# Performance work log

Hardware: AMD Instinct MI355X
Metric: run time of the kernel (lower is better)

The kernel has to match this reference:

```python
import jax, jax.numpy as jnp
import numpy as np

N = 50000   # input nodes per graph
M = 50000   # output nodes per graph
E = 1600000 # edges (avg degree 32)
B = 16      # batch size
D = 32      # Kaiming fan for init std


def setup_inputs() -> dict:
    key = jax.random.key(0)
    k1, k2, k3 = jax.random.split(key, 3)
    indices = jax.random.randint(k1, (2, E), 0, N, dtype=jnp.int64)  # row0=src in [0,N), row1=dst in [0,M)
    values = jax.random.normal(k2, (E,), dtype=jnp.float32) * (2.0 / D) ** 0.5
    bias = jnp.zeros((M, 1), dtype=jnp.float32)
    x = jax.random.normal(k3, (B, N, 1), dtype=jnp.float32)
    return {"x": x, "values": values, "bias": bias, "indices": indices}


def reference(x, values, bias, indices):
    # x: (B, N, 1); values: (E,); bias: (M, 1); indices: (2, E)
    # Equivalent to the PyG scatter-add message passing, but the block-diagonal
    # batched edge_index is never materialized: the sparsity pattern is shared
    # across the batch, so we gather once per batch via fancy indexing and
    # segment-sum over destination nodes.
    src, dst = indices[0], indices[1]
    msgs = x[:, src, 0] * values[None, :]                 # (B, E) gather-multiply
    agg = jax.ops.segment_sum(msgs.T, dst, num_segments=M)  # (M, B) scatter-add
    out = agg.T + bias[:, 0][None, :]                     # (B, M) bias add
    return out[..., None]                                  # (B, M, 1)
```

## Files before the change

kernel.cpp:

```cpp
#include <hip/hip_runtime.h>

#define E_EDGES 1600000
#define N_NODES 50000
#define M_NODES 50000
#define B_BATCH 16

#define RB         64
#define KB_BKT     782
#define TBLK       1024
#define NWG_T      49
#define NWG_B      512
#define CHUNK      3125
#define LD_ITERS   4
#define SLOT_CAP   8
#define BSPILL_CAP 64
#define PADR       73
#define ROW_CAP    72
#define SENT       0xFFFFFFFFu

__global__ void __launch_bounds__(TBLK) kAB6(
                     const float* __restrict__ x,
                     const int* __restrict__ idx,
                     const float* __restrict__ vals,
                     float4* __restrict__ xt,
                     float2* __restrict__ cells,
                     float2* __restrict__ bspill,
                     unsigned* __restrict__ scnt) {
    const int tid = threadIdx.x;
    if (blockIdx.x < NWG_T) {
        int n = blockIdx.x * TBLK + tid;
        if (n >= N_NODES) return;
        float v[B_BATCH];
#pragma unroll
        for (int b = 0; b < B_BATCH; ++b) v[b] = x[(size_t)b * N_NODES + n];
        float4* dst = xt + (size_t)n * 4;
#pragma unroll
        for (int j = 0; j < 4; ++j)
            dst[j] = make_float4(v[4*j], v[4*j+1], v[4*j+2], v[4*j+3]);
        return;
    }
    const int w = blockIdx.x - NWG_T;

    __shared__ unsigned cur[KB_BKT];
    __shared__ float2 cellbuf[KB_BKT * SLOT_CAP];

    for (int i = tid; i < KB_BKT; i += TBLK) cur[i] = 0;
    const float2 sent = make_float2(__uint_as_float(SENT), 0.f);
    for (int i = tid; i < KB_BKT * SLOT_CAP; i += TBLK) cellbuf[i] = sent;
    __syncthreads();

    const int base = w * CHUNK;
#pragma unroll
    for (int it = 0; it < LD_ITERS; ++it) {
        int li = it * TBLK + tid;
        if (li < CHUNK) {
            int e = base + li;
            unsigned s = (unsigned)idx[e];
            unsigned d = (unsigned)idx[E_EDGES + e];
            float v = vals[e];
            unsigned k = d >> 6;
            unsigned pack = s | (d << 16);
            unsigned p = atomicAdd(&cur[k], 1u);
            if (p < SLOT_CAP) {
                cellbuf[k * SLOT_CAP + p] = make_float2(__uint_as_float(pack), v);
            } else {
                unsigned sp = atomicAdd(&scnt[k], 1u);
                if (sp < BSPILL_CAP)
                    bspill[(size_t)k * BSPILL_CAP + sp] =
                        make_float2(__uint_as_float(pack), v);
            }
        }
    }
    __syncthreads();

    float4* cellsv4 = (float4*)cells;
    const float4* lbuf = (const float4*)cellbuf;
#pragma unroll
    for (int it2 = 0; it2 < 4; ++it2) {
        int kb = it2 * 256 + ((tid >> 6) << 4) + ((tid & 63) >> 2);
        int sub = tid & 3;
        if (kb < KB_BKT)
            cellsv4[((size_t)kb * NWG_B + w) * 4 + sub] = lbuf[kb * 4 + sub];
    }
}

__global__ void kC4(const float2* __restrict__ cells,
                    const float2* __restrict__ bspill,
                    const unsigned* __restrict__ scnt,
                    const float4* __restrict__ xt,
                    const float* __restrict__ bias,
                    float* __restrict__ out) {
    __shared__ float2 rowbuf[RB * PADR];
    __shared__ unsigned rcur[RB];
    __shared__ int oflow;
    __shared__ unsigned snum;

    const int tid = threadIdx.x;
    const int k = blockIdx.x;
    const int mbase = k * RB;

    if (tid < RB) rcur[tid] = 0;
    if (tid == 0) { oflow = 0; snum = scnt[k]; }
    __syncthreads();

    const float2* bkt = cells + (size_t)k * (NWG_B * SLOT_CAP);
    for (int i = tid; i < NWG_B * SLOT_CAP; i += 256) {
        float2 ed = bkt[i];
        unsigned u = __float_as_uint(ed.x);
        if (u != SENT) {
            unsigned r = (u >> 16) & 63u;
            unsigned q = atomicAdd(&rcur[r], 1u);
            if (q < ROW_CAP) rowbuf[r * PADR + q] = ed;
            else oflow = 1;
        }
    }
    __syncthreads();

    if (snum) {
        unsigned ns = (snum > BSPILL_CAP) ? BSPILL_CAP : snum;
        if ((unsigned)tid < ns) {
            float2 ed = bspill[(size_t)k * BSPILL_CAP + tid];
            unsigned r = (__float_as_uint(ed.x) >> 16) & 63u;
            unsigned q = atomicAdd(&rcur[r], 1u);
            if (q < ROW_CAP) rowbuf[r * PADR + q] = ed;
            else oflow = 1;
        }
        __syncthreads();
    }

    if (!oflow) {
        int r = tid >> 2;
        int quad = tid & 3;
        unsigned nr = rcur[r];
        const float2* row = &rowbuf[r * PADR];
        float4 acc = make_float4(0.f, 0.f, 0.f, 0.f);
        unsigned j = 0;
        for (; j + 1 < nr; j += 2) {
            float2 a = row[j];
            float2 b = row[j + 1];
            float4 xa = xt[(size_t)(__float_as_uint(a.x) & 0xFFFFu) * 4 + quad];
            float4 xb = xt[(size_t)(__float_as_uint(b.x) & 0xFFFFu) * 4 + quad];
            acc.x += xa.x * a.y; acc.y += xa.y * a.y;
            acc.z += xa.z * a.y; acc.w += xa.w * a.y;
            acc.x += xb.x * b.y; acc.y += xb.y * b.y;
            acc.z += xb.z * b.y; acc.w += xb.w * b.y;
        }
        if (j < nr) {
            float2 a = row[j];
            float4 xa = xt[(size_t)(__float_as_uint(a.x) & 0xFFFFu) * 4 + quad];
            acc.x += xa.x * a.y; acc.y += xa.y * a.y;
            acc.z += xa.z * a.y; acc.w += xa.w * a.y;
        }
        int m = mbase + r;
        if (m < M_NODES) {
            float bv = bias[m];
            out[(size_t)(quad * 4 + 0) * M_NODES + m] = acc.x + bv;
            out[(size_t)(quad * 4 + 1) * M_NODES + m] = acc.y + bv;
            out[(size_t)(quad * 4 + 2) * M_NODES + m] = acc.z + bv;
            out[(size_t)(quad * 4 + 3) * M_NODES + m] = acc.w + bv;
        }
    } else {
        __syncthreads();
        float* acc = (float*)rowbuf;
        for (int i = tid; i < B_BATCH * RB; i += 256) acc[i] = 0.f;
        __syncthreads();
        for (int i = tid; i < NWG_B * SLOT_CAP; i += 256) {
            float2 ed = bkt[i];
            unsigned u = __float_as_uint(ed.x);
            if (u != SENT) {
                int src = (int)(u & 0xFFFFu);
                int dl = (int)((u >> 16) & 63u);
                float v = ed.y;
                const float4* xr = xt + (size_t)src * 4;
                float4 a = xr[0], b4 = xr[1], cc = xr[2], d4 = xr[3];
                float xv[B_BATCH] = {a.x,a.y,a.z,a.w, b4.x,b4.y,b4.z,b4.w,
                                     cc.x,cc.y,cc.z,cc.w, d4.x,d4.y,d4.z,d4.w};
#pragma unroll
                for (int b = 0; b < B_BATCH; ++b)
                    atomicAdd(&acc[b * RB + dl], xv[b] * v);
            }
        }
        if (snum) {
            unsigned ns = (snum > BSPILL_CAP) ? BSPILL_CAP : snum;
            if ((unsigned)tid < ns) {
                float2 ed = bspill[(size_t)k * BSPILL_CAP + tid];
                unsigned u = __float_as_uint(ed.x);
                int src = (int)(u & 0xFFFFu);
                int dl = (int)((u >> 16) & 63u);
                float v = ed.y;
                const float4* xr = xt + (size_t)src * 4;
                float4 a = xr[0], b4 = xr[1], cc = xr[2], d4 = xr[3];
                float xv[B_BATCH] = {a.x,a.y,a.z,a.w, b4.x,b4.y,b4.z,b4.w,
                                     cc.x,cc.y,cc.z,cc.w, d4.x,d4.y,d4.z,d4.w};
#pragma unroll
                for (int b = 0; b < B_BATCH; ++b)
                    atomicAdd(&acc[b * RB + dl], xv[b] * v);
            }
        }
        __syncthreads();
        for (int i = tid; i < B_BATCH * RB; i += 256) {
            int b = i >> 6;
            int dl = i & (RB - 1);
            int m = mbase + dl;
            if (m < M_NODES)
                out[(size_t)b * M_NODES + m] = acc[b * RB + dl] + bias[m];
        }
    }
}


__global__ void sl2_init_bias(const float* __restrict__ bias, float* __restrict__ out) {
    int m = blockIdx.x * blockDim.x + threadIdx.x;
    if (m < M_NODES) {
        float bv = bias[m];
#pragma unroll
        for (int b = 0; b < B_BATCH; ++b) out[(size_t)b * M_NODES + m] = bv;
    }
}

__global__ void sl2_edge_scatter(const float* __restrict__ x,
                                 const float* __restrict__ vals,
                                 const int* __restrict__ idx,
                                 float* __restrict__ out) {
    int e = blockIdx.x * blockDim.x + threadIdx.x;
    if (e >= E_EDGES) return;
    int src = idx[e];
    int dst = idx[E_EDGES + e];
    float v = vals[e];
    float xv[B_BATCH];
#pragma unroll
    for (int b = 0; b < B_BATCH; ++b) xv[b] = x[(size_t)b * N_NODES + src];
#pragma unroll
    for (int b = 0; b < B_BATCH; ++b)
        unsafeAtomicAdd(&out[(size_t)b * M_NODES + dst], xv[b] * v);
}


extern "C" void kernel_launch(void* const* d_in, const int* in_sizes, int n_in,
                              void* d_out, int out_size, void* d_ws, size_t ws_size,
                              hipStream_t stream) {
    const float* x    = (const float*)d_in[0];
    const float* vals = (const float*)d_in[1];
    const float* bias = (const float*)d_in[2];
    const int*   idx  = (const int*)d_in[3];
    float* out = (float*)d_out;

    const size_t xt_bytes = (size_t)N_NODES * B_BATCH * sizeof(float);
    const size_t cl_bytes = (size_t)KB_BKT * NWG_B * SLOT_CAP * sizeof(float2);
    const size_t sp_bytes = (size_t)KB_BKT * BSPILL_CAP * sizeof(float2);
    const size_t sc_bytes = ((size_t)KB_BKT * sizeof(unsigned) + 255) & ~255ull;
    const size_t need = xt_bytes + cl_bytes + sp_bytes + sc_bytes;

    if (ws_size >= need) {
        char* p = (char*)d_ws;
        float4*   xt     = (float4*)p;    p += xt_bytes;
        float2*   cells  = (float2*)p;    p += cl_bytes;
        float2*   bspill = (float2*)p;    p += sp_bytes;
        unsigned* scnt   = (unsigned*)p;

        hipMemsetAsync(scnt, 0, (size_t)KB_BKT * sizeof(unsigned), stream);
        kAB6<<<NWG_T + NWG_B, TBLK, 0, stream>>>(x, idx, vals, xt, cells, bspill, scnt);
        kC4<<<KB_BKT, 256, 0, stream>>>(cells, bspill, scnt, xt, bias, out);
    } else {
        sl2_init_bias<<<(M_NODES + 255) / 256, 256, 0, stream>>>(bias, out);
        sl2_edge_scatter<<<(E_EDGES + 255) / 256, 256, 0, stream>>>(x, vals, idx, out);
    }
}
```

Before: 45.59 us.

## Store bucket cells workgroup-major and stop reading at first empty slot

The intermediate cell buffer changes from bucket-major to workgroup-major layout. The producer kernel can now write its whole LDS cell buffer as one contiguous float4 copy, and the consumer kernel reads each workgroup's 8-slot cell with strided float4 loads. The consumer stops at the first sentinel slot, so empty slots are no longer read or tested. The tradeoff is that consumer reads are scattered across workgroups (64B per cell at a stride of KB_BKT cells), which may hurt coalescing compared with the previous contiguous per-bucket reads.

```diff
diff --git a/kernel.cpp b/kernel.cpp
--- a/kernel.cpp
+++ b/kernel.cpp
@@ -13,12 +13,13 @@
 #define CHUNK      3125
 #define LD_ITERS   4
 #define SLOT_CAP   8
+#define CELL_F4    (KB_BKT * SLOT_CAP / 2)
 #define BSPILL_CAP 64
 #define PADR       73
 #define ROW_CAP    72
 #define SENT       0xFFFFFFFFu
 
-__global__ void __launch_bounds__(TBLK) kAB6(
+__global__ void __launch_bounds__(TBLK) kAB8(
                      const float* __restrict__ x,
                      const int* __restrict__ idx,
                      const float* __restrict__ vals,
@@ -73,18 +74,13 @@
     }
     __syncthreads();
 
-    float4* cellsv4 = (float4*)cells;
+    float4* dstv4 = (float4*)cells + (size_t)w * CELL_F4;
     const float4* lbuf = (const float4*)cellbuf;
-#pragma unroll
-    for (int it2 = 0; it2 < 4; ++it2) {
-        int kb = it2 * 256 + ((tid >> 6) << 4) + ((tid & 63) >> 2);
-        int sub = tid & 3;
-        if (kb < KB_BKT)
-            cellsv4[((size_t)kb * NWG_B + w) * 4 + sub] = lbuf[kb * 4 + sub];
-    }
-}
-
-__global__ void kC4(const float2* __restrict__ cells,
+    for (int i = tid; i < CELL_F4; i += TBLK)
+        dstv4[i] = lbuf[i];
+}
+
+__global__ void kC6(const float2* __restrict__ cells,
                     const float2* __restrict__ bspill,
                     const unsigned* __restrict__ scnt,
                     const float4* __restrict__ xt,
@@ -103,15 +99,29 @@
     if (tid == 0) { oflow = 0; snum = scnt[k]; }
     __syncthreads();
 
-    const float2* bkt = cells + (size_t)k * (NWG_B * SLOT_CAP);
-    for (int i = tid; i < NWG_B * SLOT_CAP; i += 256) {
-        float2 ed = bkt[i];
-        unsigned u = __float_as_uint(ed.x);
-        if (u != SENT) {
-            unsigned r = (u >> 16) & 63u;
-            unsigned q = atomicAdd(&rcur[r], 1u);
-            if (q < ROW_CAP) rowbuf[r * PADR + q] = ed;
-            else oflow = 1;
+#pragma unroll
+    for (int m = 0; m < 2; ++m) {
+        int w = tid + m * 256;
+        const float4* cell = (const float4*)(cells + ((size_t)w * KB_BKT + k) * SLOT_CAP);
+#pragma unroll
+        for (int j = 0; j < 4; ++j) {
+            float4 q = cell[j];
+            unsigned u0 = __float_as_uint(q.x);
+            if (u0 == SENT) break;
+            {
+                unsigned r = (u0 >> 16) & 63u;
+                unsigned p = atomicAdd(&rcur[r], 1u);
+                if (p < ROW_CAP) rowbuf[r * PADR + p] = make_float2(q.x, q.y);
+                else oflow = 1;
+            }
+            unsigned u1 = __float_as_uint(q.z);
+            if (u1 == SENT) break;
+            {
+                unsigned r = (u1 >> 16) & 63u;
+                unsigned p = atomicAdd(&rcur[r], 1u);
+                if (p < ROW_CAP) rowbuf[r * PADR + p] = make_float2(q.z, q.w);
+                else oflow = 1;
+            }
         }
     }
     __syncthreads();
@@ -121,8 +131,8 @@
         if ((unsigned)tid < ns) {
             float2 ed = bspill[(size_t)k * BSPILL_CAP + tid];
             unsigned r = (__float_as_uint(ed.x) >> 16) & 63u;
-            unsigned q = atomicAdd(&rcur[r], 1u);
-            if (q < ROW_CAP) rowbuf[r * PADR + q] = ed;
+            unsigned p = atomicAdd(&rcur[r], 1u);
+            if (p < ROW_CAP) rowbuf[r * PADR + p] = ed;
             else oflow = 1;
         }
         __syncthreads();
@@ -164,10 +174,14 @@
         float* acc = (float*)rowbuf;
         for (int i = tid; i < B_BATCH * RB; i += 256) acc[i] = 0.f;
         __syncthreads();
-        for (int i = tid; i < NWG_B * SLOT_CAP; i += 256) {
-            float2 ed = bkt[i];
-            unsigned u = __float_as_uint(ed.x);
-            if (u != SENT) {
+#pragma unroll
+        for (int m = 0; m < 2; ++m) {
+            int w = tid + m * 256;
+            const float2* cell = cells + ((size_t)w * KB_BKT + k) * SLOT_CAP;
+            for (int j = 0; j < SLOT_CAP; ++j) {
+                float2 ed = cell[j];
+                unsigned u = __float_as_uint(ed.x);
+                if (u == SENT) break;
                 int src = (int)(u & 0xFFFFu);
                 int dl = (int)((u >> 16) & 63u);
                 float v = ed.y;
@@ -246,7 +260,7 @@
     float* out = (float*)d_out;
 
     const size_t xt_bytes = (size_t)N_NODES * B_BATCH * sizeof(float);
-    const size_t cl_bytes = (size_t)KB_BKT * NWG_B * SLOT_CAP * sizeof(float2);
+    const size_t cl_bytes = (size_t)NWG_B * KB_BKT * SLOT_CAP * sizeof(float2);
     const size_t sp_bytes = (size_t)KB_BKT * BSPILL_CAP * sizeof(float2);
     const size_t sc_bytes = ((size_t)KB_BKT * sizeof(unsigned) + 255) & ~255ull;
     const size_t need = xt_bytes + cl_bytes + sp_bytes + sc_bytes;
@@ -259,8 +273,8 @@
         unsigned* scnt   = (unsigned*)p;
 
         hipMemsetAsync(scnt, 0, (size_t)KB_BKT * sizeof(unsigned), stream);
-        kAB6<<<NWG_T + NWG_B, TBLK, 0, stream>>>(x, idx, vals, xt, cells, bspill, scnt);
-        kC4<<<KB_BKT, 256, 0, stream>>>(cells, bspill, scnt, xt, bias, out);
+        kAB8<<<NWG_T + NWG_B, TBLK, 0, stream>>>(x, idx, vals, xt, cells, bspill, scnt);
+        kC6<<<KB_BKT, 256, 0, stream>>>(cells, bspill, scnt, xt, bias, out);
     } else {
         sl2_init_bias<<<(M_NODES + 255) / 256, 256, 0, stream>>>(bias, out);
         sl2_edge_scatter<<<(E_EDGES + 255) / 256, 256, 0, stream>>>(x, vals, idx, out);
```

New measurement: 49.92 us. 9.5% more time.
